# Kernel optimization log

Measured on AMD Instinct MI355X. Metric: run time of the kernel, lower is better.

Reference implementation:

```python
import jax, jax.numpy as jnp
from jax import lax
import numpy as np

D_MODEL = 768
D_STATE = 16
D_CONV = 4
EXPAND = 2
D_INNER = EXPAND * D_MODEL
BATCH = 2
SEQ = 512


def setup_inputs() -> dict:
    key = jax.random.key(0)
    ks = jax.random.split(key, 8)
    s = 0.02
    return {
        "x": jax.random.normal(ks[0], (BATCH, SEQ, D_MODEL), jnp.float32),
        "W_in": jax.random.normal(ks[1], (2 * D_INNER, D_MODEL), jnp.float32) * s,
        "conv_w": jax.random.normal(ks[2], (D_INNER, 1, D_CONV), jnp.float32) * s,
        "conv_b": jnp.zeros((D_INNER,), jnp.float32),
        "W_x": jax.random.normal(ks[3], (D_INNER + 2 * D_STATE, D_INNER), jnp.float32) * s,
        "W_dt": jax.random.normal(ks[4], (D_INNER, D_INNER), jnp.float32) * s,
        "b_dt": jnp.zeros((D_INNER,), jnp.float32),
        "A_log": jnp.log(jax.random.uniform(ks[5], (D_INNER, D_STATE), jnp.float32, 1e-4, 1.0)),
        "Dp": jnp.ones((D_INNER,), jnp.float32),
        "W_out": jax.random.normal(ks[6], (D_MODEL, D_INNER), jnp.float32) * s,
    }


def parallel_scan_log(log_coeffs, log_values):
    """Faithful port of ParallelScan.parallel_scan_log (Blelchh-style up/down sweep
    in log space). Indices are static, so the Python loop over O(log L) levels is
    trace-time only."""
    B, L, D = log_coeffs.shape
    if L <= 4:
        run = log_values[:, 0]
        outs = [run]
        for i in range(1, L):
            run = jnp.logaddexp(run, log_coeffs[:, i] + log_values[:, i])
            outs.append(run)
        return jnp.stack(outs, axis=1)
    levels = int(np.ceil(np.log2(L)))
    coeffs, values = log_coeffs, log_values
    # up-sweep
    for level in range(levels):
        step = 2 ** (level + 1)
        if step - 1 >= L:
            break
        right = np.arange(step - 1, L, step)
        left = right - 2 ** level
        m = (left >= 0) & (right < L)
        left, right = left[m], right[m]
        if left.size == 0:
            continue
        new_c = coeffs[:, left] + coeffs[:, right]
        new_v = jnp.logaddexp(values[:, left], coeffs[:, right] + values[:, right])
        coeffs = coeffs.at[:, right].set(new_c)
        values = values.at[:, right].set(new_v)
    # down-sweep
    for level in range(levels - 1, -1, -1):
        step = 2 ** (level + 1)
        if step - 1 >= L:
            continue
        right = np.arange(step - 1, L, step)
        left = right - 2 ** level
        m = (left >= 0) & (right < L)
        left, right = left[m], right[m]
        if left.size == 0:
            continue
        tmp = values[:, right]
        new_r = jnp.logaddexp(values[:, left], coeffs[:, right] + values[:, right])
        values = values.at[:, right].set(new_r)
        values = values.at[:, left].set(tmp)
    return values


def reference(x, W_in, conv_w, conv_b, W_x, W_dt, b_dt, A_log, Dp, W_out):
    Bsz, L, _ = x.shape
    xz = x @ W_in.T                                 # [B, L, 2*d_inner]
    x_inner, z = jnp.split(xz, 2, axis=-1)
    # depthwise causal conv1d (pad left d_conv-1, truncate to L == torch slice)
    xc = jnp.transpose(x_inner, (0, 2, 1))          # [B, d_inner, L]
    xc = lax.conv_general_dilated(
        xc, conv_w, (1,), [(D_CONV - 1, 0)],
        dimension_numbers=("NCH", "OIH", "NCH"),
        feature_group_count=D_INNER)
    xc = xc + conv_b[None, :, None]
    x_conv = jax.nn.silu(jnp.transpose(xc, (0, 2, 1)))  # [B, L, d_inner]
    x_dbl = x_conv @ W_x.T                              # [B, L, d_inner + 2*d_state]
    delta, Bmat, Cmat = jnp.split(x_dbl, [D_INNER, D_INNER + D_STATE], axis=-1)
    delta = jax.nn.softplus(delta @ W_dt.T + b_dt)      # [B, L, d_inner]
    # selective scan
    A = -jnp.exp(A_log)                                 # [d_inner, d_state]
    deltaA = jnp.exp(jnp.einsum("bld,dn->bldn", delta, A))
    deltaB_u = jnp.einsum("bld,bln,bld->bldn", delta, Bmat, x_conv)
    log_coeffs = jnp.log(deltaA + 1e-12).reshape(Bsz, L, -1)
    log_values = jnp.log(jnp.abs(deltaB_u) + 1e-12).reshape(Bsz, L, -1)
    scanned = jnp.exp(parallel_scan_log(log_coeffs, log_values))
    scanned = scanned.reshape(Bsz, L, D_INNER, D_STATE)
    y = jnp.einsum("bldn,bln->bld", scanned, Cmat) + x_conv * Dp
    y = y * jax.nn.silu(z)
    return y @ W_out.T
```

## Files before the change

kernel.cpp:

```cpp
#include <hip/hip_runtime.h>
#include <math.h>

#define D_MODEL 768
#define D_STATE 16
#define D_CONV  4
#define D_INNER 1536
#define BATCH   2
#define SEQ     512
#define M_ROWS  (BATCH * SEQ)
#define N_XZ    (2 * D_INNER)
#define N_XDBL  (D_INNER + 2 * D_STATE)

typedef _Float16 half8 __attribute__((ext_vector_type(8)));
typedef float  f32x4  __attribute__((ext_vector_type(4)));
typedef unsigned short ushort_t;
typedef ushort_t ushort8_t __attribute__((ext_vector_type(8)));

__device__ __forceinline__ ushort_t f2h(float f) {
    _Float16 h = (_Float16)f;
    return *(ushort_t*)&h;
}
__device__ __forceinline__ void pack8(const float* s, ushort_t* d) {
    ushort8_t o;
#pragma unroll
    for (int j = 0; j < 8; ++j) o[j] = f2h(s[j]);
    *(ushort8_t*)d = o;
}
__device__ __forceinline__ void gld16(const ushort_t* g, void* l) {
    __builtin_amdgcn_global_load_lds((const __attribute__((address_space(1))) void*)g,
                                     (__attribute__((address_space(3))) void*)l, 16, 0, 0);
}

#define SX   (M_ROWS * D_MODEL)
#define SW1  (N_XZ * D_MODEL)
#define SW2  (N_XDBL * D_INNER)
#define SWDT (D_INNER * D_INNER)
#define SWO  (D_MODEL * D_INNER)
#define SPACK (SX + SW1 + SW2 + SWDT + SWO)
__global__ __launch_bounds__(256) void pack_kernel(
    const float* __restrict__ x, const float* __restrict__ win,
    const float* __restrict__ wx, const float* __restrict__ wdt,
    const float* __restrict__ wo,
    ushort_t* __restrict__ xs, ushort_t* __restrict__ w1, ushort_t* __restrict__ w2,
    ushort_t* __restrict__ wdt16, ushort_t* __restrict__ wo16)
{
    long i = ((long)blockIdx.x * 256 + threadIdx.x) * 8;
    if (i >= SPACK) return;
    const float* src; ushort_t* dst; long base;
    if (i < SX)                         { src = x;   dst = xs;    base = i; }
    else if (i < SX + SW1)              { src = win; dst = w1;    base = i - SX; }
    else if (i < SX + SW1 + SW2)        { src = wx;  dst = w2;    base = i - SX - SW1; }
    else if (i < SX + SW1 + SW2 + SWDT) { src = wdt; dst = wdt16; base = i - SX - SW1 - SW2; }
    else                                { src = wo;  dst = wo16;  base = i - SX - SW1 - SW2 - SWDT; }
    float v[8];
    *(float4*)(v)     = *(const float4*)(src + base);
    *(float4*)(v + 4) = *(const float4*)(src + base + 4);
    pack8(v, dst + base);
}

__global__ __launch_bounds__(512) void gemm_lds(
    const ushort_t* __restrict__ A, int lda,
    const ushort_t* __restrict__ B, int ldb,
    float* __restrict__ Cbase, long pstride, int ldc,
    int N, int kc)
{
    __shared__ ushort_t smA[3][4096];
    __shared__ ushort_t smB[3][4096];

    const int tid  = threadIdx.x;
    const int w    = tid >> 6;
    const int lane = tid & 63;
    const int lr   = lane & 15;
    const int lq   = lane >> 4;

    const int Gx = gridDim.x, Gy = gridDim.y;
    const int T = Gx * Gy * gridDim.z;
    const int f = blockIdx.x + Gx * (blockIdx.y + Gy * blockIdx.z);
    const int g = (T & 7) ? f : ((f & 7) * (T >> 3) + (f >> 3));
    const int bx = g % Gx;
    const int by = (g / Gx) % Gy;
    const int z  = g / (Gx * Gy);
    float* __restrict__ C = Cbase + (long)z * pstride;

    const int bm = by * 128;
    const int bn = bx * 128;
    const int k0base = z * kc;

    auto stage = [&](int buf, int k0) {
        {
            const int rA = bm + w * 16 + lr;
            gld16(A + (long)rA * lda + k0 + lq * 8, &smA[buf][w * 512]);
        }
        {
            int rB = bn + w * 16 + lr; if (rB >= N) rB = N - 1;
            gld16(B + (long)rB * ldb + k0 + lq * 8, &smB[buf][w * 512]);
        }
    };

    f32x4 acc[4][2] = {};
    const int wm = (w & 1) * 64;
    const int wn = (w >> 1) * 32;

    const int nIter = kc >> 5;
    stage(0, k0base);
    int cur = 0;
    for (int it = 0; it < nIter; ++it) {
        const int nxt = (cur == 2) ? 0 : cur + 1;
        if (it + 1 < nIter) {
            stage(nxt, k0base + (it + 1) * 32);
            asm volatile("s_waitcnt vmcnt(2)" ::: "memory");
        } else {
            asm volatile("s_waitcnt vmcnt(0)" ::: "memory");
        }
        __builtin_amdgcn_s_barrier();
        asm volatile("" ::: "memory");

        half8 ah[4], bh[2];
#pragma unroll
        for (int mt = 0; mt < 4; ++mt)
            ah[mt] = *(const half8*)&smA[cur][(((w & 1) * 4 + mt) * 512) + lq * 128 + lr * 8];
#pragma unroll
        for (int nt = 0; nt < 2; ++nt)
            bh[nt] = *(const half8*)&smB[cur][(((w >> 1) * 2 + nt) * 512) + lq * 128 + lr * 8];
#pragma unroll
        for (int mt = 0; mt < 4; ++mt)
#pragma unroll
            for (int nt = 0; nt < 2; ++nt)
                acc[mt][nt] = __builtin_amdgcn_mfma_f32_16x16x32_f16(ah[mt], bh[nt], acc[mt][nt], 0, 0, 0);
        cur = nxt;
    }

#pragma unroll
    for (int mt = 0; mt < 4; ++mt)
#pragma unroll
        for (int nt = 0; nt < 2; ++nt)
#pragma unroll
            for (int r = 0; r < 4; ++r) {
                int row = bm + wm + mt * 16 + lq * 4 + r;
                int col = bn + wn + nt * 16 + lr;
                if (col >= N) continue;
                C[(long)row * ldc + col] = acc[mt][nt][r];
            }
}

__global__ __launch_bounds__(256) void conv_silu_kernel(
    const float* __restrict__ p0, const float* __restrict__ p1,
    const float* __restrict__ conv_w, const float* __restrict__ conv_b,
    float* __restrict__ xconvT, float* __restrict__ zsiluT,
    ushort_t* __restrict__ xc)
{
    __shared__ float Tx[64][17];
    __shared__ float Tz[64][17];
    const int rb = blockIdx.x;
    const int db = blockIdx.y;
    const int dl = threadIdx.x & 63;
    const int d  = db * 64 + dl;
    const int rr = threadIdx.x >> 6;
    const float w0 = conv_w[d * 4 + 0], w1 = conv_w[d * 4 + 1];
    const float w2 = conv_w[d * 4 + 2], w3 = conv_w[d * 4 + 3];
    const float bb = conv_b[d];
#pragma unroll
    for (int q = 0; q < 4; ++q) {
        const int r = rb * 16 + q * 4 + rr;
        const int l = r & (SEQ - 1);
        float acc = bb;
        if (l >= 3) { long o = (long)(r - 3) * N_XZ + d; acc = fmaf(w0, p0[o] + p1[o], acc); }
        if (l >= 2) { long o = (long)(r - 2) * N_XZ + d; acc = fmaf(w1, p0[o] + p1[o], acc); }
        if (l >= 1) { long o = (long)(r - 1) * N_XZ + d; acc = fmaf(w2, p0[o] + p1[o], acc); }
        { long o = (long)r * N_XZ + d; acc = fmaf(w3, p0[o] + p1[o], acc); }
        float s = acc / (1.f + expf(-acc));
        xc[(long)r * D_INNER + d] = f2h(s);
        long oz = (long)r * N_XZ + D_INNER + d;
        float zv = p0[oz] + p1[oz];
        Tx[dl][q * 4 + rr] = s;
        Tz[dl][q * 4 + rr] = zv / (1.f + expf(-zv));
    }
    __syncthreads();
    const int rp = threadIdx.x & 15;
    const int dp = threadIdx.x >> 4;
#pragma unroll
    for (int p = 0; p < 4; ++p) {
        int dd = p * 16 + dp;
        long o = (long)(db * 64 + dd) * M_ROWS + rb * 16 + rp;
        xconvT[o] = Tx[dd][rp];
        zsiluT[o] = Tz[dd][rp];
    }
}

__global__ __launch_bounds__(256) void ep_xdbl_kernel(
    const float* __restrict__ P, long ps,
    ushort_t* __restrict__ xd, float* __restrict__ BCT)
{
    long i = ((long)blockIdx.x * 256 + threadIdx.x) * 8;
    if (i >= (long)M_ROWS * N_XDBL) return;
    int row = (int)(i / N_XDBL);
    int col = (int)(i - (long)row * N_XDBL);
    float f[8];
#pragma unroll
    for (int j = 0; j < 8; ++j) f[j] = P[i + j] + P[i + j + ps] + P[i + j + 2 * ps];
    pack8(f, xd + i);
    if (col >= D_INNER) {
#pragma unroll
        for (int j = 0; j < 8; ++j)
            BCT[(long)(col + j - D_INNER) * M_ROWS + row] = f[j];
    }
}

__global__ __launch_bounds__(256) void ep_merge_kernel(
    const float* __restrict__ P, long ps, float* __restrict__ out)
{
    long i = ((long)blockIdx.x * 256 + threadIdx.x) * 8;
    if (i >= (long)M_ROWS * D_MODEL) return;
    float o[8];
#pragma unroll
    for (int j = 0; j < 8; ++j) {
        float v = 0.f;
#pragma unroll
        for (int z = 0; z < 6; ++z) v += P[i + j + z * ps];
        o[j] = v;
    }
    *(float4*)(out + i)     = *(float4*)(o);
    *(float4*)(out + i + 4) = *(float4*)(o + 4);
}

__global__ __launch_bounds__(256) void scan_kernel(
    const float* __restrict__ P, long ps,
    const float* __restrict__ b_dt,
    const float* __restrict__ xconvT,
    const float* __restrict__ zsiluT,
    const float* __restrict__ BCT,
    const float* __restrict__ A_log,
    const float* __restrict__ Dp,
    float* __restrict__ uT)
{
    __shared__ float dlT[512];
    __shared__ float xrT[512];
    __shared__ float red[3 * 512];

    const int bid = blockIdx.x;
    const int b   = bid / D_INNER;
    const int d   = bid % D_INNER;
    const int tid = threadIdx.x;
    const int w   = tid >> 6;
    const int t   = tid & 63;
    const long od = (long)d * M_ROWS + b * SEQ;

    const float bdt = b_dt[d];
#pragma unroll
    for (int q = 0; q < 2; ++q) {
        const int l = tid + q * 256;
        float v = P[od + l] + P[od + l + ps] + P[od + l + 2 * ps] + P[od + l + 3 * ps] + bdt;
        float sp = fmaxf(v, 0.f) + log1pf(expf(-fabsf(v)));
        const int li = (l & 7) * 64 + (l >> 3);
        dlT[li] = sp;
        xrT[li] = xconvT[od + l];
    }
    __syncthreads();

    float dl[8], xr[8], dx[8], yac[8];
#pragma unroll
    for (int j = 0; j < 8; ++j) {
        dl[j] = dlT[j * 64 + t];
        xr[j] = xrT[j * 64 + t];
        dx[j] = dl[j] * xr[j];
        yac[j] = 0.f;
    }
    const int l0 = 8 * t;

#pragma unroll
    for (int nn = 0; nn < 4; ++nn) {
        const int n = w * 4 + nn;
        const float Adn = -expf(A_log[d * D_STATE + n]);
        const float4* Bp = (const float4*)(BCT + (long)n * M_ROWS + b * SEQ + l0);
        float4 b0 = Bp[0], b1 = Bp[1];
        float Bv[8] = {b0.x, b0.y, b0.z, b0.w, b1.x, b1.y, b1.z, b1.w};
        float c[8], v[8];
#pragma unroll
        for (int j = 0; j < 8; ++j) {
            c[j] = __expf(dl[j] * Adn);
            v[j] = fabsf(dx[j] * Bv[j]);
        }
        float c01 = c[1] * c[0], v01 = fmaf(c[1], v[0], v[1]);
        float c23 = c[3] * c[2], v23 = fmaf(c[3], v[2], v[3]);
        float c45 = c[5] * c[4], v45 = fmaf(c[5], v[4], v[5]);
        float c67 = c[7] * c[6], v67 = fmaf(c[7], v[6], v[7]);
        float c03 = c23 * c01,  v03 = fmaf(c23, v01, v23);
        float c47 = c67 * c45,  v47 = fmaf(c67, v45, v67);
        float cA  = c47 * c03,  vA  = fmaf(c47, v03, v47);
#pragma unroll
        for (int h = 1; h <= 32; h <<= 1) {
            float cl = __shfl_up(cA, (unsigned)h);
            float vl = __shfl_up(vA, (unsigned)h);
            if (t >= h) { vA = fmaf(cA, vl, vA); cA = cA * cl; }
        }
        float s = __shfl_up(vA, 1u);
        if (t == 0) s = 0.f;
        const float4* Cp = (const float4*)(BCT + (long)(16 + n) * M_ROWS + b * SEQ + l0);
        float4 c0 = Cp[0], c1 = Cp[1];
        float Cv[8] = {c0.x, c0.y, c0.z, c0.w, c1.x, c1.y, c1.z, c1.w};
#pragma unroll
        for (int j = 0; j < 8; ++j) {
            s = fmaf(c[j], s, v[j]);
            yac[j] = fmaf(s, Cv[j], yac[j]);
        }
    }

    if (w) {
#pragma unroll
        for (int j = 0; j < 8; ++j) red[(w - 1) * 512 + j * 64 + t] = yac[j];
    }
    __syncthreads();
    if (w == 0) {
        const float Dpd = Dp[d];
#pragma unroll
        for (int j = 0; j < 8; ++j) {
            float y = yac[j] + red[j * 64 + t] + red[512 + j * 64 + t] + red[1024 + j * 64 + t];
            float uv = fmaf(xr[j], Dpd, y) * zsiluT[od + l0 + j];
            uT[od + l0 + j] = uv;
        }
    }
}

__global__ __launch_bounds__(256) void transpose_split_kernel(
    const float* __restrict__ uT, ushort_t* __restrict__ u)
{
    __shared__ float T[64][65];
    const int m0 = blockIdx.x * 64;
    const int d0 = blockIdx.y * 64;
    const int c  = threadIdx.x & 63;
    const int rr = threadIdx.x >> 6;
#pragma unroll
    for (int p = 0; p < 64; p += 4)
        T[p + rr][c] = uT[(long)(d0 + p + rr) * M_ROWS + m0 + c];
    __syncthreads();
#pragma unroll
    for (int p = 0; p < 64; p += 4) {
        int rm = p + rr;
        float v = T[c][rm];
        u[(long)(m0 + rm) * D_INNER + (d0 + c)] = f2h(v);
    }
}

extern "C" void kernel_launch(void* const* d_in, const int* in_sizes, int n_in,
                              void* d_out, int out_size, void* d_ws, size_t ws_size,
                              hipStream_t stream)
{
    (void)in_sizes; (void)n_in; (void)out_size; (void)ws_size;

    const float* x      = (const float*)d_in[0];
    const float* W_in   = (const float*)d_in[1];
    const float* conv_w = (const float*)d_in[2];
    const float* conv_b = (const float*)d_in[3];
    const float* W_x    = (const float*)d_in[4];
    const float* W_dt   = (const float*)d_in[5];
    const float* b_dt   = (const float*)d_in[6];
    const float* A_log  = (const float*)d_in[7];
    const float* Dp     = (const float*)d_in[8];
    const float* W_out  = (const float*)d_in[9];
    float* out = (float*)d_out;

    float* ws = (float*)d_ws;
    long off = 0;
    float* P      = ws + off; off += 2L * M_ROWS * N_XZ;
    float* xconvT = ws + off; off += (long)D_INNER * M_ROWS;
    float* zsiluT = ws + off; off += (long)D_INNER * M_ROWS;
    float* uT     = ws + off; off += (long)D_INNER * M_ROWS;
    float* xsbuf  = ws + off; off += (long)M_ROWS * D_MODEL / 2;
    float* w1buf  = ws + off; off += (long)N_XZ * D_MODEL / 2;
    float* w2buf  = ws + off; off += (long)N_XDBL * D_INNER / 2;
    float* wdtbuf = ws + off; off += (long)D_INNER * D_INNER / 2;
    float* wobuf  = ws + off; off += (long)D_MODEL * D_INNER / 2;
    float* xcbuf  = ws + off; off += (long)M_ROWS * D_INNER / 2;
    float* xdbuf  = ws + off; off += (long)M_ROWS * N_XDBL / 2;
    float* BCT    = ws + off; off += (long)2 * D_STATE * M_ROWS;

    ushort_t* xs    = (ushort_t*)xsbuf;
    ushort_t* w1    = (ushort_t*)w1buf;
    ushort_t* w2    = (ushort_t*)w2buf;
    ushort_t* wdt16 = (ushort_t*)wdtbuf;
    ushort_t* wo16  = (ushort_t*)wobuf;
    ushort_t* xc    = (ushort_t*)xcbuf;
    ushort_t* xd    = (ushort_t*)xdbuf;
    ushort_t* u_i   = (ushort_t*)xcbuf;
    float* P6       = P;

    const long psG4 = (long)D_INNER * M_ROWS;

    dim3 blk(256);
    dim3 gblk(512);

    pack_kernel<<<dim3(SPACK / 2048), blk, 0, stream>>>(
        x, W_in, W_x, W_dt, W_out, xs, w1, w2, wdt16, wo16);
    gemm_lds<<<dim3(N_XZ / 128, M_ROWS / 128, 2), gblk, 0, stream>>>(
        xs, D_MODEL, w1, D_MODEL, P, (long)M_ROWS * N_XZ, N_XZ, N_XZ, D_MODEL / 2);
    conv_silu_kernel<<<dim3(M_ROWS / 16, D_INNER / 64), blk, 0, stream>>>(
        P, P + (long)M_ROWS * N_XZ, conv_w, conv_b, xconvT, zsiluT, xc);
    gemm_lds<<<dim3((N_XDBL + 127) / 128, M_ROWS / 128, 3), gblk, 0, stream>>>(
        xc, D_INNER, w2, D_INNER, P, (long)M_ROWS * N_XDBL, N_XDBL, N_XDBL, D_INNER / 3);
    ep_xdbl_kernel<<<dim3((M_ROWS * N_XDBL) / 2048), blk, 0, stream>>>(
        P, (long)M_ROWS * N_XDBL, xd, BCT);
    gemm_lds<<<dim3(M_ROWS / 128, D_INNER / 128, 4), gblk, 0, stream>>>(
        wdt16, D_INNER, xd, N_XDBL, P, psG4, M_ROWS, M_ROWS, D_INNER / 4);
    scan_kernel<<<dim3(BATCH * D_INNER), blk, 0, stream>>>(
        P, psG4, b_dt, xconvT, zsiluT, BCT, A_log, Dp, uT);
    transpose_split_kernel<<<dim3(M_ROWS / 64, D_INNER / 64), blk, 0, stream>>>(
        uT, u_i);
    gemm_lds<<<dim3(D_MODEL / 128, M_ROWS / 128, 6), gblk, 0, stream>>>(
        u_i, D_INNER, wo16, D_INNER, P6, (long)M_ROWS * D_MODEL, D_MODEL, D_MODEL, D_INNER / 6);
    ep_merge_kernel<<<dim3((M_ROWS * D_MODEL) / 2048), blk, 0, stream>>>(
        P6, (long)M_ROWS * D_MODEL, out);
}
```

Baseline: 203.6 us.

## Store split-K GEMM partials and scan output in fp16 to halve traffic

Three of the four GEMMs now write their split-K partial sums as fp16 instead of fp32, and the consumers (conv_silu, scan, ep_merge) read and widen them to float. The scan output uT is also stored as fp16 with vectorized 8-wide writes, and the transpose kernel moves halves instead of converting. The goal is to halve intermediate memory traffic between stages. The cost is extra rounding on partial sums before they are reduced, which adds accuracy risk.

After: 202.4 us, median of 2. Within noise of the previous version (-0.6%).

```diff
diff --git a/kernel.cpp b/kernel.cpp
--- a/kernel.cpp
+++ b/kernel.cpp
@@ -19,6 +19,9 @@
 __device__ __forceinline__ ushort_t f2h(float f) {
     _Float16 h = (_Float16)f;
     return *(ushort_t*)&h;
+}
+__device__ __forceinline__ float h2f(ushort_t u) {
+    return (float)(*(const _Float16*)&u);
 }
 __device__ __forceinline__ void pack8(const float* s, ushort_t* d) {
     ushort8_t o;
@@ -58,10 +61,11 @@
     pack8(v, dst + base);
 }
 
+template<int HALF_OUT>
 __global__ __launch_bounds__(512) void gemm_lds(
     const ushort_t* __restrict__ A, int lda,
     const ushort_t* __restrict__ B, int ldb,
-    float* __restrict__ Cbase, long pstride, int ldc,
+    void* __restrict__ Cbase, long pstride, int ldc,
     int N, int kc)
 {
     __shared__ ushort_t smA[3][4096];
@@ -80,7 +84,8 @@
     const int bx = g % Gx;
     const int by = (g / Gx) % Gy;
     const int z  = g / (Gx * Gy);
-    float* __restrict__ C = Cbase + (long)z * pstride;
+    ushort_t* __restrict__ Ch = (ushort_t*)Cbase + (long)z * pstride;
+    float*    __restrict__ Cf = (float*)Cbase + (long)z * pstride;
 
     const int bm = by * 128;
     const int bn = bx * 128;
@@ -139,12 +144,13 @@
                 int row = bm + wm + mt * 16 + lq * 4 + r;
                 int col = bn + wn + nt * 16 + lr;
                 if (col >= N) continue;
-                C[(long)row * ldc + col] = acc[mt][nt][r];
+                if (HALF_OUT) Ch[(long)row * ldc + col] = f2h(acc[mt][nt][r]);
+                else          Cf[(long)row * ldc + col] = acc[mt][nt][r];
             }
 }
 
 __global__ __launch_bounds__(256) void conv_silu_kernel(
-    const float* __restrict__ p0, const float* __restrict__ p1,
+    const ushort_t* __restrict__ p0, const ushort_t* __restrict__ p1,
     const float* __restrict__ conv_w, const float* __restrict__ conv_b,
     float* __restrict__ xconvT, float* __restrict__ zsiluT,
     ushort_t* __restrict__ xc)
@@ -164,14 +170,14 @@
         const int r = rb * 16 + q * 4 + rr;
         const int l = r & (SEQ - 1);
         float acc = bb;
-        if (l >= 3) { long o = (long)(r - 3) * N_XZ + d; acc = fmaf(w0, p0[o] + p1[o], acc); }
-        if (l >= 2) { long o = (long)(r - 2) * N_XZ + d; acc = fmaf(w1, p0[o] + p1[o], acc); }
-        if (l >= 1) { long o = (long)(r - 1) * N_XZ + d; acc = fmaf(w2, p0[o] + p1[o], acc); }
-        { long o = (long)r * N_XZ + d; acc = fmaf(w3, p0[o] + p1[o], acc); }
+        if (l >= 3) { long o = (long)(r - 3) * N_XZ + d; acc = fmaf(w0, h2f(p0[o]) + h2f(p1[o]), acc); }
+        if (l >= 2) { long o = (long)(r - 2) * N_XZ + d; acc = fmaf(w1, h2f(p0[o]) + h2f(p1[o]), acc); }
+        if (l >= 1) { long o = (long)(r - 1) * N_XZ + d; acc = fmaf(w2, h2f(p0[o]) + h2f(p1[o]), acc); }
+        { long o = (long)r * N_XZ + d; acc = fmaf(w3, h2f(p0[o]) + h2f(p1[o]), acc); }
         float s = acc / (1.f + expf(-acc));
         xc[(long)r * D_INNER + d] = f2h(s);
         long oz = (long)r * N_XZ + D_INNER + d;
-        float zv = p0[oz] + p1[oz];
+        float zv = h2f(p0[oz]) + h2f(p1[oz]);
         Tx[dl][q * 4 + rr] = s;
         Tz[dl][q * 4 + rr] = zv / (1.f + expf(-zv));
     }
@@ -207,31 +213,30 @@
 }
 
 __global__ __launch_bounds__(256) void ep_merge_kernel(
-    const float* __restrict__ P, long ps, float* __restrict__ out)
+    const ushort_t* __restrict__ P, long ps, float* __restrict__ out)
 {
     long i = ((long)blockIdx.x * 256 + threadIdx.x) * 8;
     if (i >= (long)M_ROWS * D_MODEL) return;
-    float o[8];
-#pragma unroll
-    for (int j = 0; j < 8; ++j) {
-        float v = 0.f;
-#pragma unroll
-        for (int z = 0; z < 6; ++z) v += P[i + j + z * ps];
-        o[j] = v;
+    float o[8] = {};
+#pragma unroll
+    for (int z = 0; z < 6; ++z) {
+        ushort8_t v = *(const ushort8_t*)(P + i + z * ps);
+#pragma unroll
+        for (int j = 0; j < 8; ++j) o[j] += h2f(v[j]);
     }
     *(float4*)(out + i)     = *(float4*)(o);
     *(float4*)(out + i + 4) = *(float4*)(o + 4);
 }
 
 __global__ __launch_bounds__(256) void scan_kernel(
-    const float* __restrict__ P, long ps,
+    const ushort_t* __restrict__ P, long ps,
     const float* __restrict__ b_dt,
     const float* __restrict__ xconvT,
     const float* __restrict__ zsiluT,
     const float* __restrict__ BCT,
     const float* __restrict__ A_log,
     const float* __restrict__ Dp,
-    float* __restrict__ uT)
+    ushort_t* __restrict__ uT)
 {
     __shared__ float dlT[512];
     __shared__ float xrT[512];
@@ -249,7 +254,8 @@
 #pragma unroll
     for (int q = 0; q < 2; ++q) {
         const int l = tid + q * 256;
-        float v = P[od + l] + P[od + l + ps] + P[od + l + 2 * ps] + P[od + l + 3 * ps] + bdt;
+        float v = h2f(P[od + l]) + h2f(P[od + l + ps]) + h2f(P[od + l + 2 * ps])
+                + h2f(P[od + l + 3 * ps]) + bdt;
         float sp = fmaxf(v, 0.f) + log1pf(expf(-fabsf(v)));
         const int li = (l & 7) * 64 + (l >> 3);
         dlT[li] = sp;
@@ -312,19 +318,21 @@
     __syncthreads();
     if (w == 0) {
         const float Dpd = Dp[d];
+        ushort8_t uo;
 #pragma unroll
         for (int j = 0; j < 8; ++j) {
             float y = yac[j] + red[j * 64 + t] + red[512 + j * 64 + t] + red[1024 + j * 64 + t];
             float uv = fmaf(xr[j], Dpd, y) * zsiluT[od + l0 + j];
-            uT[od + l0 + j] = uv;
-        }
+            uo[j] = f2h(uv);
+        }
+        *(ushort8_t*)(uT + od + l0) = uo;
     }
 }
 
 __global__ __launch_bounds__(256) void transpose_split_kernel(
-    const float* __restrict__ uT, ushort_t* __restrict__ u)
-{
-    __shared__ float T[64][65];
+    const ushort_t* __restrict__ uT, ushort_t* __restrict__ u)
+{
+    __shared__ ushort_t T[64][65];
     const int m0 = blockIdx.x * 64;
     const int d0 = blockIdx.y * 64;
     const int c  = threadIdx.x & 63;
@@ -336,8 +344,7 @@
 #pragma unroll
     for (int p = 0; p < 64; p += 4) {
         int rm = p + rr;
-        float v = T[c][rm];
-        u[(long)(m0 + rm) * D_INNER + (d0 + c)] = f2h(v);
+        u[(long)(m0 + rm) * D_INNER + (d0 + c)] = T[c][rm];
     }
 }
 
@@ -364,7 +371,7 @@
     float* P      = ws + off; off += 2L * M_ROWS * N_XZ;
     float* xconvT = ws + off; off += (long)D_INNER * M_ROWS;
     float* zsiluT = ws + off; off += (long)D_INNER * M_ROWS;
-    float* uT     = ws + off; off += (long)D_INNER * M_ROWS;
+    float* uTbuf  = ws + off; off += (long)D_INNER * M_ROWS / 2;
     float* xsbuf  = ws + off; off += (long)M_ROWS * D_MODEL / 2;
     float* w1buf  = ws + off; off += (long)N_XZ * D_MODEL / 2;
     float* w2buf  = ws + off; off += (long)N_XDBL * D_INNER / 2;
@@ -382,31 +389,34 @@
     ushort_t* xc    = (ushort_t*)xcbuf;
     ushort_t* xd    = (ushort_t*)xdbuf;
     ushort_t* u_i   = (ushort_t*)xcbuf;
-    float* P6       = P;
+    ushort_t* uT    = (ushort_t*)uTbuf;
+    ushort_t* P16   = (ushort_t*)P;
 
     const long psG4 = (long)D_INNER * M_ROWS;
+    const long psG1 = (long)M_ROWS * N_XZ;
+    const long psG6 = (long)M_ROWS * D_MODEL;
 
     dim3 blk(256);
     dim3 gblk(512);
 
     pack_kernel<<<dim3(SPACK / 2048), blk, 0, stream>>>(
         x, W_in, W_x, W_dt, W_out, xs, w1, w2, wdt16, wo16);
-    gemm_lds<<<dim3(N_XZ / 128, M_ROWS / 128, 2), gblk, 0, stream>>>(
-        xs, D_MODEL, w1, D_MODEL, P, (long)M_ROWS * N_XZ, N_XZ, N_XZ, D_MODEL / 2);
+    gemm_lds<1><<<dim3(N_XZ / 128, M_ROWS / 128, 2), gblk, 0, stream>>>(
+        xs, D_MODEL, w1, D_MODEL, P16, psG1, N_XZ, N_XZ, D_MODEL / 2);
     conv_silu_kernel<<<dim3(M_ROWS / 16, D_INNER / 64), blk, 0, stream>>>(
-        P, P + (long)M_ROWS * N_XZ, conv_w, conv_b, xconvT, zsiluT, xc);
-    gemm_lds<<<dim3((N_XDBL + 127) / 128, M_ROWS / 128, 3), gblk, 0, stream>>>(
+        P16, P16 + psG1, conv_w, conv_b, xconvT, zsiluT, xc);
+    gemm_lds<0><<<dim3((N_XDBL + 127) / 128, M_ROWS / 128, 3), gblk, 0, stream>>>(
         xc, D_INNER, w2, D_INNER, P, (long)M_ROWS * N_XDBL, N_XDBL, N_XDBL, D_INNER / 3);
     ep_xdbl_kernel<<<dim3((M_ROWS * N_XDBL) / 2048), blk, 0, stream>>>(
         P, (long)M_ROWS * N_XDBL, xd, BCT);
-    gemm_lds<<<dim3(M_ROWS / 128, D_INNER / 128, 4), gblk, 0, stream>>>(
-        wdt16, D_INNER, xd, N_XDBL, P, psG4, M_ROWS, M_ROWS, D_INNER / 4);
+    gemm_lds<1><<<dim3(M_ROWS / 128, D_INNER / 128, 4), gblk, 0, stream>>>(
+        wdt16, D_INNER, xd, N_XDBL, P16, psG4, M_ROWS, M_ROWS, D_INNER / 4);
     scan_kernel<<<dim3(BATCH * D_INNER), blk, 0, stream>>>(
-        P, psG4, b_dt, xconvT, zsiluT, BCT, A_log, Dp, uT);
+        P16, psG4, b_dt, xconvT, zsiluT, BCT, A_log, Dp, uT);
     transpose_split_kernel<<<dim3(M_ROWS / 64, D_INNER / 64), blk, 0, stream>>>(
         uT, u_i);
-    gemm_lds<<<dim3(D_MODEL / 128, M_ROWS / 128, 6), gblk, 0, stream>>>(
-        u_i, D_INNER, wo16, D_INNER, P6, (long)M_ROWS * D_MODEL, D_MODEL, D_MODEL, D_INNER / 6);
+    gemm_lds<1><<<dim3(D_MODEL / 128, M_ROWS / 128, 6), gblk, 0, stream>>>(
+        u_i, D_INNER, wo16, D_INNER, P16, psG6, D_MODEL, D_MODEL, D_INNER / 6);
     ep_merge_kernel<<<dim3((M_ROWS * D_MODEL) / 2048), blk, 0, stream>>>(
-        P6, (long)M_ROWS * D_MODEL, out);
-}
+        P16, psG6, out);
+}
```
